# Optimization experiments

Measured on AMD Instinct MI355X. Metric: run time of the kernel, lower is better.

The kernel has to match this reference:

```python
import jax, jax.numpy as jnp
import numpy as np

N = 200000          # num nodes (num_rus)
E = 12800000        # num edges (avg degree 64)
IN_C, HID, OUT = 1, 16, 4


def setup_inputs() -> dict:
    key = jax.random.key(0)
    ks = jax.random.split(key, 6)
    x = jax.random.normal(ks[0], (N, IN_C), dtype=jnp.float32)
    edges = jax.random.randint(ks[1], (2, E), 0, N, dtype=jnp.int64)
    W1 = jax.random.normal(ks[2], (IN_C, HID), dtype=jnp.float32) / np.sqrt(IN_C)
    b1 = jnp.zeros((HID,), dtype=jnp.float32)
    W2 = jax.random.normal(ks[3], (HID, HID), dtype=jnp.float32) / np.sqrt(HID)
    b2 = jnp.zeros((HID,), dtype=jnp.float32)
    Wl = jax.random.normal(ks[4], (HID, OUT), dtype=jnp.float32) / np.sqrt(HID)
    bl = jnp.zeros((OUT,), dtype=jnp.float32)
    return {"x": x, "edges": edges, "W1": W1, "b1": b1, "W2": W2, "b2": b2, "Wl": Wl, "bl": bl}


def _gcn_norm(edges):
    # PyG GCNConv default: add self-loops, symmetric normalization.
    loops = jnp.arange(N, dtype=edges.dtype)
    src = jnp.concatenate([edges[0], loops])   # [E+N]
    dst = jnp.concatenate([edges[1], loops])
    deg = jax.ops.segment_sum(jnp.ones_like(dst, dtype=jnp.float32), dst, num_segments=N)
    dinv = jnp.where(deg > 0, jax.lax.rsqrt(deg), 0.0)
    norm = dinv[src] * dinv[dst]               # [E+N]
    return src, dst, norm


def _gcn_conv(h, W, b, src, dst, norm):
    m = h @ W                                  # [N, out] transform first (cheap, small C)
    msgs = m[src] * norm[:, None]              # gather + normalize, [E+N, out]
    agg = jax.ops.segment_sum(msgs, dst, num_segments=N)
    return agg + b


def reference(x, edges, W1, b1, W2, b2, Wl, bl):
    src, dst, norm = _gcn_norm(edges)
    h = jax.nn.relu(_gcn_conv(x, W1, b1, src, dst, norm))
    h = jax.nn.relu(_gcn_conv(h, W2, b2, src, dst, norm))
    return h @ Wl + bl                         # [N, 4]
```

## Files before the change

### kernel.cpp

```cpp
#include <hip/hip_runtime.h>

#define HID 16
#define OUTC 4
#define G 64
#define SBSH 8
#define SBN 256
#define CAP 21504
#define PHSH 16
#define SUBK 8
#define KB (SBN * SUBK)
#define PBLK 512
#define NPB_MAX 800
#define NPB_H 400
#define STCAP 46
#define STP 47
#define EPB 16
#define EPP (PBLK * EPB)
#define SENT 0xFFFFFFFFu

__device__ __forceinline__ float relu(float v) { return v > 0.f ? v : 0.f; }

__global__ void k_cnt(const int* __restrict__ dst, int* __restrict__ cnt,
                      int E, int nsb, int nc, int ncsh) {
    __shared__ int lc[NPB_MAX];
    for (int i = threadIdx.x; i < nsb; i += PBLK) lc[i] = 0;
    __syncthreads();
    int c = blockIdx.x;
    int chunk = (E + nc - 1) / nc;
    int lo = c * chunk, hi = lo + chunk < E ? lo + chunk : E;
    for (int i = lo + threadIdx.x; i < hi; i += PBLK)
        atomicAdd(lc + (dst[i] >> SBSH), 1);
    __syncthreads();
    for (int b = threadIdx.x; b < nsb; b += PBLK)
        cnt[(b << ncsh) + c] = (lc[b] + 15) & ~15;
}

__global__ void k_scanA(int* __restrict__ a, int* __restrict__ bsum, int L) {
    __shared__ int s[1024];
    int i = blockIdx.x * 1024 + threadIdx.x;
    int v = (i < L) ? a[i] : 0;
    s[threadIdx.x] = v; __syncthreads();
    for (int off = 1; off < 1024; off <<= 1) {
        int t = (threadIdx.x >= (unsigned)off) ? s[threadIdx.x - off] : 0;
        __syncthreads();
        s[threadIdx.x] += t;
        __syncthreads();
    }
    if (i < L) a[i] = s[threadIdx.x] - v;
    if (threadIdx.x == 1023) bsum[blockIdx.x] = s[1023];
}

__global__ void k_scanB(int* __restrict__ bsum, int SB) {
    __shared__ int s[1024];
    int carry = 0;
    for (int base = 0; base < SB; base += 1024) {
        int idx = base + threadIdx.x;
        int v = (idx < SB) ? bsum[idx] : 0;
        s[threadIdx.x] = v; __syncthreads();
        for (int off = 1; off < 1024; off <<= 1) {
            int t = (threadIdx.x >= (unsigned)off) ? s[threadIdx.x - off] : 0;
            __syncthreads();
            s[threadIdx.x] += t;
            __syncthreads();
        }
        if (idx < SB) bsum[idx] = carry + s[threadIdx.x] - v;
        carry += s[1023];
        __syncthreads();
    }
    if (threadIdx.x == 0) bsum[SB] = carry;
}

__global__ void k_scanC(int* __restrict__ a, const int* __restrict__ bsum,
                        int* __restrict__ bOff, int L, int nsb, int SB,
                        int nc, int ncsh) {
    int i = blockIdx.x * 1024 + threadIdx.x;
    if (i < L) {
        int v = a[i] + bsum[blockIdx.x];
        a[i] = v;
        if ((i & (nc - 1)) == 0) bOff[i >> ncsh] = v;
    }
    if (blockIdx.x == 0 && threadIdx.x == 0) bOff[nsb] = bsum[SB];
}

__global__ void __launch_bounds__(PBLK) k_part(const int* __restrict__ src,
                                               const int* __restrict__ dst,
                                               const int* __restrict__ cnt,
                                               unsigned int* __restrict__ rec,
                                               int E, int nsb, int nc, int ncsh) {
    __shared__ unsigned int stage[NPB_H * STP];
    __shared__ int scnt[NPB_H];
    __shared__ int gcur[NPB_H];
    int c = blockIdx.x >> 1, h = blockIdx.x & 1;
    int nh = (nsb - h + 1) >> 1;
    for (int bh = threadIdx.x; bh < nh; bh += PBLK) {
        scnt[bh] = 0;
        gcur[bh] = cnt[((bh * 2 + h) << ncsh) + c];
    }
    __syncthreads();
    int chunk = (E + nc - 1) / nc;
    int lo = c * chunk, hi = lo + chunk < E ? lo + chunk : E;
    for (int base = lo; base < hi; base += EPP) {
#pragma unroll 4
        for (int k = 0; k < EPB; ++k) {
            int i = base + k * PBLK + threadIdx.x;
            if (i < hi) {
                int d = dst[i], s = src[i];
                int b = d >> SBSH;
                if ((b & 1) == h) {
                    int bh = b >> 1;
                    int pos = atomicAdd(scnt + bh, 1);
                    if (pos < STCAP)
                        stage[bh * STP + pos] = (unsigned int)s | ((unsigned int)(d & (SBN - 1)) << 18);
                }
            }
        }
        __syncthreads();
        for (int bh = threadIdx.x; bh < nh; bh += PBLK) {
            int n = scnt[bh];
            int f = n & ~15;
            if (f > 0) {
                uint4* d4 = (uint4*)&rec[gcur[bh]];
                const unsigned int* sp0 = &stage[bh * STP];
                for (int j = 0; j < f; j += 16) {
                    const unsigned int* sp = sp0 + j;
                    d4[0] = make_uint4(sp[0], sp[1], sp[2], sp[3]);
                    d4[1] = make_uint4(sp[4], sp[5], sp[6], sp[7]);
                    d4[2] = make_uint4(sp[8], sp[9], sp[10], sp[11]);
                    d4[3] = make_uint4(sp[12], sp[13], sp[14], sp[15]);
                    d4 += 4;
                }
                gcur[bh] += f;
                for (int j = 0; j < n - f; ++j) stage[bh * STP + j] = stage[bh * STP + f + j];
                scnt[bh] = n - f;
            }
        }
        __syncthreads();
    }
    for (int bh = threadIdx.x; bh < nh; bh += PBLK) {
        int n = scnt[bh];
        if (n > 0) {
            unsigned int tmp[16];
            for (int j = 0; j < 16; ++j) tmp[j] = (j < n) ? stage[bh * STP + j] : SENT;
            uint4* d4 = (uint4*)&rec[gcur[bh]];
            d4[0] = make_uint4(tmp[0], tmp[1], tmp[2], tmp[3]);
            d4[1] = make_uint4(tmp[4], tmp[5], tmp[6], tmp[7]);
            d4[2] = make_uint4(tmp[8], tmp[9], tmp[10], tmp[11]);
            d4[3] = make_uint4(tmp[12], tmp[13], tmp[14], tmp[15]);
        }
    }
}

__global__ void __launch_bounds__(256) k_sort(const int* __restrict__ bOff,
                                              unsigned int* __restrict__ rec,
                                              float* __restrict__ dinv,
                                              int* __restrict__ rowp,
                                              int N, int nsb, int E) {
    __shared__ unsigned int raw[CAP];
    __shared__ int hist[KB], cur[KB];
    __shared__ int s[256];
    int b = blockIdx.x;
    int beg = bOff[b], end = bOff[b + 1];
    int size = end - beg; if (size > CAP) size = CAP;
    for (int i = threadIdx.x; i < size; i += 256) raw[i] = rec[beg + i];
    for (int k = threadIdx.x; k < KB; k += 256) hist[k] = 0;
    __syncthreads();
    for (int i = threadIdx.x; i < size; i += 256) {
        unsigned int r = raw[i];
        if (r == SENT) continue;
        int key = (int)((r >> 18) << 3) | (int)((r & 0x3FFFF) >> PHSH);
        atomicAdd(hist + key, 1);
    }
    __syncthreads();
    int t = threadIdx.x;
    int psum = 0;
#pragma unroll
    for (int j = 0; j < SUBK; ++j) psum += hist[t * SUBK + j];
    s[t] = psum; __syncthreads();
    for (int off = 1; off < 256; off <<= 1) {
        int v = (t >= off) ? s[t - off] : 0;
        __syncthreads();
        s[t] += v;
        __syncthreads();
    }
    int ex = s[t] - psum;
    {
        int n = b * SBN + t;
        bool valid = (n < N);
        int running = ex;
#pragma unroll
        for (int j = 0; j < SUBK; ++j) {
            cur[t * SUBK + j] = running;
            if (valid) rowp[(size_t)n * SUBK + j] = beg + running;
            running += hist[t * SUBK + j];
        }
        if (valid) dinv[n] = rsqrtf((float)psum + 1.0f);
    }
    __syncthreads();
    for (int i = t; i < size; i += 256) {
        unsigned int r = raw[i];
        if (r == SENT) continue;
        int key = (int)((r >> 18) << 3) | (int)((r & 0x3FFFF) >> PHSH);
        int p = atomicAdd(cur + key, 1);
        rec[beg + p] = r & 0x3FFFF;
    }
}

__global__ void k_m1(const float* __restrict__ x, const float* __restrict__ W1,
                     const float* __restrict__ dinv, float* __restrict__ m, int N) {
    int t = blockIdx.x * blockDim.x + threadIdx.x;
    if (t < N * HID) {
        int n = t >> 4, c = t & 15;
        m[t] = x[n] * W1[c] * dinv[n];
    }
}

__global__ void k_m2(float4* __restrict__ h4, const float* __restrict__ W2,
                     const float* __restrict__ dinv, int N) {
    __shared__ float hs[64][HID + 1];
    __shared__ float w[HID * HID];
    if (threadIdx.x < HID * HID) w[threadIdx.x] = W2[threadIdx.x];
    int idx = blockIdx.x * 256 + threadIdx.x;
    int n = idx >> 2, q = idx & 3;
    int ln = threadIdx.x >> 2;
    if (n < N) {
        float4 v = h4[idx];
        hs[ln][q * 4 + 0] = v.x; hs[ln][q * 4 + 1] = v.y;
        hs[ln][q * 4 + 2] = v.z; hs[ln][q * 4 + 3] = v.w;
    }
    __syncthreads();
    if (n < N) {
        float dn = dinv[n];
        float4 acc = make_float4(0.f, 0.f, 0.f, 0.f);
        const float* hr = hs[ln];
#pragma unroll
        for (int ci = 0; ci < HID; ++ci) {
            float hv = hr[ci];
            const float* wr = w + ci * HID + q * 4;
            acc.x += hv * wr[0]; acc.y += hv * wr[1];
            acc.z += hv * wr[2]; acc.w += hv * wr[3];
        }
        acc.x *= dn; acc.y *= dn; acc.z *= dn; acc.w *= dn;
        h4[idx] = acc;
    }
}

template <int MODE>
__global__ void __launch_bounds__(256) k_aggp(const int* __restrict__ rowp,
                                              const unsigned int* __restrict__ adj,
                                              const float* __restrict__ dinv,
                                              const float4* __restrict__ mS4,
                                              float4* __restrict__ gagg4,
                                              const float4* __restrict__ b4,
                                              const float* __restrict__ Wl,
                                              const float* __restrict__ bl,
                                              float* __restrict__ out,
                                              int N, int p) {
    __shared__ float hs[G][HID + 1];
    __shared__ float wl[HID * OUTC];
    __shared__ float blv[OUTC];
    if (MODE == 2) {
        if (threadIdx.x < HID * OUTC) wl[threadIdx.x] = Wl[threadIdx.x];
        if (threadIdx.x < OUTC) blv[threadIdx.x] = bl[threadIdx.x];
    }
    int dl = threadIdx.x >> 2, q = threadIdx.x & 3;
    int n = blockIdx.x * G + dl;
    if (n < N) {
        int i = rowp[(size_t)n * SUBK + p];
        int end = rowp[(size_t)n * SUBK + p + 1];
        float4 acc = (p == 0) ? mS4[n * 4 + q] : gagg4[n * 4 + q];
        for (; i + 4 <= end; i += 4) {
            int s0 = adj[i] * 4 + q, s1 = adj[i + 1] * 4 + q;
            int s2 = adj[i + 2] * 4 + q, s3 = adj[i + 3] * 4 + q;
            float4 v0 = mS4[s0], v1 = mS4[s1], v2 = mS4[s2], v3 = mS4[s3];
            acc.x += v0.x + v1.x + v2.x + v3.x;
            acc.y += v0.y + v1.y + v2.y + v3.y;
            acc.z += v0.z + v1.z + v2.z + v3.z;
            acc.w += v0.w + v1.w + v2.w + v3.w;
        }
        for (; i < end; ++i) {
            float4 v = mS4[adj[i] * 4 + q];
            acc.x += v.x; acc.y += v.y; acc.z += v.z; acc.w += v.w;
        }
        if (MODE == 0) {
            gagg4[n * 4 + q] = acc;
        } else {
            float dn = dinv[n];
            float4 bb = b4[q];
            float4 h;
            h.x = relu(acc.x * dn + bb.x);
            h.y = relu(acc.y * dn + bb.y);
            h.z = relu(acc.z * dn + bb.z);
            h.w = relu(acc.w * dn + bb.w);
            if (MODE == 1) {
                gagg4[n * 4 + q] = h;
            } else {
                hs[dl][q * 4 + 0] = h.x; hs[dl][q * 4 + 1] = h.y;
                hs[dl][q * 4 + 2] = h.z; hs[dl][q * 4 + 3] = h.w;
            }
        }
    }
    if (MODE == 2) {
        __syncthreads();
        if (n < N) {
            float acc = blv[q];
            const float* hr = hs[dl];
#pragma unroll
            for (int ci = 0; ci < HID; ++ci) acc += hr[ci] * wl[ci * OUTC + q];
            out[n * OUTC + q] = acc;
        }
    }
}

static inline size_t alignup(size_t v, size_t a) { return (v + a - 1) & ~(a - 1); }

extern "C" void kernel_launch(void* const* d_in, const int* in_sizes, int n_in,
                              void* d_out, int out_size, void* d_ws, size_t ws_size,
                              hipStream_t stream) {
    const float* x  = (const float*)d_in[0];
    const int* ed   = (const int*)d_in[1];
    const float* W1 = (const float*)d_in[2];
    const float* b1 = (const float*)d_in[3];
    const float* W2 = (const float*)d_in[4];
    const float* b2 = (const float*)d_in[5];
    const float* Wl = (const float*)d_in[6];
    const float* bl = (const float*)d_in[7];
    float* out      = (float*)d_out;

    int N = in_sizes[0];
    int E = in_sizes[1] / 2;
    const int* src = ed;
    const int* dst = ed + E;
    int nsb = (N + SBN - 1) / SBN;
    int nb64 = (N + G - 1) / G;
    int nphase = (N + (1 << PHSH) - 1) >> PHSH;

    int nc = 256, ncsh = 8;
    size_t o = 0;
    float* dinv; int* rowp; int* bsum; int* bOff; unsigned int* rec;
    float* bufA; float* bufB;
    char* w = (char*)d_ws;
    for (int attempt = 0; attempt < 2; ++attempt) {
        int L = nsb * nc;
        int SB = (L + 1023) / 1024;
        size_t Epad = (size_t)E + 15 * (size_t)L;
        o = 0;
        dinv = (float*)(w + o); o = alignup(o + (size_t)N * 4, 64);
        rowp = (int*)(w + o);   o = alignup(o + (size_t)N * SUBK * 4, 64);
        bsum = (int*)(w + o);   o = alignup(o + ((size_t)SB + 1) * 4, 64);
        bOff = (int*)(w + o);   o = alignup(o + ((size_t)nsb + 1) * 4, 64);
        rec  = (unsigned int*)(w + o); o = alignup(o + Epad * 4, 64);
        bufA = (float*)(w + o); o = alignup(o + (size_t)N * HID * 4, 64);
        bufB = (float*)(w + o); o = alignup(o + (size_t)N * HID * 4, 64);
        if (o <= ws_size || nc == 128) break;
        nc = 128; ncsh = 7;
    }
    int L = nsb * nc;
    int SB = (L + 1023) / 1024;
    int* cnt = (int*)bufA;

    int blk = 256;
    int gN16 = (N * HID + blk - 1) / blk;

    k_cnt<<<nc, PBLK, 0, stream>>>(dst, cnt, E, nsb, nc, ncsh);
    k_scanA<<<SB, 1024, 0, stream>>>(cnt, bsum, L);
    k_scanB<<<1, 1024, 0, stream>>>(bsum, SB);
    k_scanC<<<SB, 1024, 0, stream>>>(cnt, bsum, bOff, L, nsb, SB, nc, ncsh);
    k_part<<<nc * 2, PBLK, 0, stream>>>(src, dst, cnt, rec, E, nsb, nc, ncsh);
    k_sort<<<nsb, 256, 0, stream>>>(bOff, rec, dinv, rowp, N, nsb, E);

    k_m1<<<gN16, blk, 0, stream>>>(x, W1, dinv, bufA, N);
    for (int p = 0; p < nphase; ++p) {
        if (p < nphase - 1)
            k_aggp<0><<<nb64, blk, 0, stream>>>(rowp, rec, dinv, (const float4*)bufA,
                                                (float4*)bufB, (const float4*)b1,
                                                nullptr, nullptr, nullptr, N, p);
        else
            k_aggp<1><<<nb64, blk, 0, stream>>>(rowp, rec, dinv, (const float4*)bufA,
                                                (float4*)bufB, (const float4*)b1,
                                                nullptr, nullptr, nullptr, N, p);
    }

    k_m2<<<nb64, blk, 0, stream>>>((float4*)bufB, W2, dinv, N);
    for (int p = 0; p < nphase; ++p) {
        if (p < nphase - 1)
            k_aggp<0><<<nb64, blk, 0, stream>>>(rowp, rec, dinv, (const float4*)bufB,
                                                (float4*)bufA, (const float4*)b2,
                                                nullptr, nullptr, nullptr, N, p);
        else
            k_aggp<2><<<nb64, blk, 0, stream>>>(rowp, rec, dinv, (const float4*)bufB,
                                                (float4*)bufA, (const float4*)b2,
                                                Wl, bl, out, N, p);
    }
}
```

Before: 560.3 us.

## Unroll count/sort/gather loops and split staging flush across four threads

The count and sort histogram/scatter loops are unrolled four ways. The sort kernel now loads records with uint4 vector copies. The partition flush gives each bucket to a group of four threads, each writing one uint4, instead of one thread writing all of them. The gather loop gains an 8-wide unrolled path so more independent loads are in flight. Together these aim at more memory-level parallelism and fewer serial flush loops, at the cost of more registers. The uint4 raw load assumes the segment size and base offset are multiples of 4, which the 16-padding appears to guarantee.

```diff
diff --git a/kernel.cpp b/kernel.cpp
--- a/kernel.cpp
+++ b/kernel.cpp
@@ -28,8 +28,13 @@
     int c = blockIdx.x;
     int chunk = (E + nc - 1) / nc;
     int lo = c * chunk, hi = lo + chunk < E ? lo + chunk : E;
-    for (int i = lo + threadIdx.x; i < hi; i += PBLK)
-        atomicAdd(lc + (dst[i] >> SBSH), 1);
+    for (int i = lo + threadIdx.x; i < hi; i += PBLK * 4) {
+#pragma unroll
+        for (int u = 0; u < 4; ++u) {
+            int ii = i + u * PBLK;
+            if (ii < hi) atomicAdd(lc + (dst[ii] >> SBSH), 1);
+        }
+    }
     __syncthreads();
     for (int b = threadIdx.x; b < nsb; b += PBLK)
         cnt[(b << ncsh) + c] = (lc[b] + 15) & ~15;
@@ -99,6 +104,7 @@
     __syncthreads();
     int chunk = (E + nc - 1) / nc;
     int lo = c * chunk, hi = lo + chunk < E ? lo + chunk : E;
+    int g4 = threadIdx.x >> 2, r4 = threadIdx.x & 3;
     for (int base = lo; base < hi; base += EPP) {
 #pragma unroll 4
         for (int k = 0; k < EPB; ++k) {
@@ -115,23 +121,21 @@
             }
         }
         __syncthreads();
-        for (int bh = threadIdx.x; bh < nh; bh += PBLK) {
+        for (int bh = g4; bh < nh; bh += PBLK / 4) {
             int n = scnt[bh];
             int f = n & ~15;
             if (f > 0) {
-                uint4* d4 = (uint4*)&rec[gcur[bh]];
-                const unsigned int* sp0 = &stage[bh * STP];
+                int gc = gcur[bh];
                 for (int j = 0; j < f; j += 16) {
-                    const unsigned int* sp = sp0 + j;
-                    d4[0] = make_uint4(sp[0], sp[1], sp[2], sp[3]);
-                    d4[1] = make_uint4(sp[4], sp[5], sp[6], sp[7]);
-                    d4[2] = make_uint4(sp[8], sp[9], sp[10], sp[11]);
-                    d4[3] = make_uint4(sp[12], sp[13], sp[14], sp[15]);
-                    d4 += 4;
+                    const unsigned int* sp = &stage[bh * STP + j] + r4 * 4;
+                    ((uint4*)&rec[gc + j])[r4] = make_uint4(sp[0], sp[1], sp[2], sp[3]);
                 }
-                gcur[bh] += f;
-                for (int j = 0; j < n - f; ++j) stage[bh * STP + j] = stage[bh * STP + f + j];
-                scnt[bh] = n - f;
+                if (r4 == 0) {
+                    gcur[bh] = gc + f;
+                    for (int jj = 0; jj < n - f; ++jj)
+                        stage[bh * STP + jj] = stage[bh * STP + f + jj];
+                    scnt[bh] = n - f;
+                }
             }
         }
         __syncthreads();
@@ -161,14 +165,26 @@
     int b = blockIdx.x;
     int beg = bOff[b], end = bOff[b + 1];
     int size = end - beg; if (size > CAP) size = CAP;
-    for (int i = threadIdx.x; i < size; i += 256) raw[i] = rec[beg + i];
+    {
+        uint4* raw4 = (uint4*)raw;
+        const uint4* rec4 = (const uint4*)&rec[beg];
+        int size4 = size >> 2;
+        for (int i = threadIdx.x; i < size4; i += 256) raw4[i] = rec4[i];
+    }
     for (int k = threadIdx.x; k < KB; k += 256) hist[k] = 0;
     __syncthreads();
-    for (int i = threadIdx.x; i < size; i += 256) {
-        unsigned int r = raw[i];
-        if (r == SENT) continue;
-        int key = (int)((r >> 18) << 3) | (int)((r & 0x3FFFF) >> PHSH);
-        atomicAdd(hist + key, 1);
+    for (int i = threadIdx.x; i < size; i += 1024) {
+#pragma unroll
+        for (int u = 0; u < 4; ++u) {
+            int ii = i + u * 256;
+            if (ii < size) {
+                unsigned int r = raw[ii];
+                if (r != SENT) {
+                    int key = (int)((r >> 18) << 3) | (int)((r & 0x3FFFF) >> PHSH);
+                    atomicAdd(hist + key, 1);
+                }
+            }
+        }
     }
     __syncthreads();
     int t = threadIdx.x;
@@ -196,12 +212,19 @@
         if (valid) dinv[n] = rsqrtf((float)psum + 1.0f);
     }
     __syncthreads();
-    for (int i = t; i < size; i += 256) {
-        unsigned int r = raw[i];
-        if (r == SENT) continue;
-        int key = (int)((r >> 18) << 3) | (int)((r & 0x3FFFF) >> PHSH);
-        int p = atomicAdd(cur + key, 1);
-        rec[beg + p] = r & 0x3FFFF;
+    for (int i = t; i < size; i += 1024) {
+#pragma unroll
+        for (int u = 0; u < 4; ++u) {
+            int ii = i + u * 256;
+            if (ii < size) {
+                unsigned int r = raw[ii];
+                if (r != SENT) {
+                    int key = (int)((r >> 18) << 3) | (int)((r & 0x3FFFF) >> PHSH);
+                    int p = atomicAdd(cur + key, 1);
+                    rec[beg + p] = r & 0x3FFFF;
+                }
+            }
+        }
     }
 }
 
@@ -268,6 +291,18 @@
         int i = rowp[(size_t)n * SUBK + p];
         int end = rowp[(size_t)n * SUBK + p + 1];
         float4 acc = (p == 0) ? mS4[n * 4 + q] : gagg4[n * 4 + q];
+        for (; i + 8 <= end; i += 8) {
+            int s0 = adj[i] * 4 + q, s1 = adj[i + 1] * 4 + q;
+            int s2 = adj[i + 2] * 4 + q, s3 = adj[i + 3] * 4 + q;
+            int s4 = adj[i + 4] * 4 + q, s5 = adj[i + 5] * 4 + q;
+            int s6 = adj[i + 6] * 4 + q, s7 = adj[i + 7] * 4 + q;
+            float4 v0 = mS4[s0], v1 = mS4[s1], v2 = mS4[s2], v3 = mS4[s3];
+            float4 v4 = mS4[s4], v5 = mS4[s5], v6 = mS4[s6], v7 = mS4[s7];
+            acc.x += (v0.x + v1.x + v2.x + v3.x) + (v4.x + v5.x + v6.x + v7.x);
+            acc.y += (v0.y + v1.y + v2.y + v3.y) + (v4.y + v5.y + v6.y + v7.y);
+            acc.z += (v0.z + v1.z + v2.z + v3.z) + (v4.z + v5.z + v6.z + v7.z);
+            acc.w += (v0.w + v1.w + v2.w + v3.w) + (v4.w + v5.w + v6.w + v7.w);
+        }
         for (; i + 4 <= end; i += 4) {
             int s0 = adj[i] * 4 + q, s1 = adj[i + 1] * 4 + q;
             int s2 = adj[i + 2] * 4 + q, s3 = adj[i + 3] * 4 + q;
```

Measured after the change: 538.2 us. 4.0% less time.
